# Kernel optimization log

Hardware: AMD Instinct MI355X
Metric: run time of the kernel (lower is better)

Reference implementation:

```python
import jax, jax.numpy as jnp
import numpy as np

DIM = 1024
HEADS = 16
ORDER = 3
B, L = 4, 1024  # note: L must equal DIM due to broadcast in original code


def setup_inputs() -> dict:
    key = jax.random.key(0)
    ks = jax.random.split(key, 10)
    D = DIM
    s = 0.02
    inp = {
        "x": jax.random.normal(ks[0], (B, L, D), dtype=jnp.float32),
        "Wq": jax.random.normal(ks[1], (D, D), dtype=jnp.float32) * s,
        "bq": jnp.zeros((D,), jnp.float32),
        "Wk": jax.random.normal(ks[2], (D, D), dtype=jnp.float32) * s,
        "bk": jnp.zeros((D,), jnp.float32),
        "Wv": jax.random.normal(ks[3], (D, D), dtype=jnp.float32) * s,
        "bv": jnp.zeros((D,), jnp.float32),
        "Wo": jax.random.normal(ks[4], (D, D), dtype=jnp.float32) * s,
        "bo": jnp.zeros((D,), jnp.float32),
        # init per module: zeros field, 0.1 strengths
        "torsion_field": jnp.zeros((ORDER, D), jnp.float32),
        "torsion_strength": jnp.ones((ORDER,), jnp.float32) * 0.1,
    }
    return inp


def reference(x, Wq, bq, Wk, bk, Wv, bv, Wo, bo, torsion_field, torsion_strength):
    Bsz, Ln, D = x.shape
    H = HEADS
    hd = D // H

    def proj(W, b):
        y = jnp.einsum('bld,ed->ble', x, W) + b  # Linear: x @ W.T + b
        return y.reshape(Bsz, Ln, H, hd).transpose(0, 2, 1, 3)  # (B,H,L,hd)

    q = proj(Wq, bq)
    k = proj(Wk, bk)
    v = proj(Wv, bv)

    scores = jnp.einsum('bhld,bhmd->bhlm', q, k) / jnp.sqrt(jnp.float32(hd))

    # torsion bias: sum_i strength_i * sin(arange(L)*(i+1)*pi/L) * sigmoid(field_i)
    # (requires L == D for the elementwise product, as in the original)
    pos = jnp.arange(Ln, dtype=jnp.float32)                       # (L,)
    orders = jnp.arange(1, ORDER + 1, dtype=jnp.float32)          # (O,)
    mods = torsion_strength[:, None] * jnp.sin(pos[None, :] * orders[:, None] * jnp.pi / Ln)  # (O,L)
    phases = jax.nn.sigmoid(torsion_field)                        # (O,D), D==L
    bias = jnp.sum(mods * phases, axis=0)                         # (L,)
    scores = scores + bias[None, None, None, :]

    torsion_energy = jnp.sum(torsion_strength ** 2) / ORDER

    attn = jax.nn.softmax(scores, axis=-1)
    out = jnp.einsum('bhlm,bhmd->bhld', attn, v)
    out = out.transpose(0, 2, 1, 3).reshape(Bsz, Ln, D)
    out = jnp.einsum('bld,ed->ble', out, Wo) + bo
    return out, attn, torsion_energy
```

## Files before the change

### kernel.cpp

```cpp
#include <hip/hip_runtime.h>
#include <hip/hip_bf16.h>

typedef __bf16 bf16x8 __attribute__((ext_vector_type(8)));
typedef float f32x4 __attribute__((ext_vector_type(4)));

#define GLDS16(gp, lp) \
    __builtin_amdgcn_global_load_lds((__attribute__((address_space(1))) void*)(gp), \
                                     (__attribute__((address_space(3))) void*)(lp), 16, 0, 0)

__global__ __launch_bounds__(256) void k_convert(
    const float* __restrict__ x, const float* __restrict__ Wq,
    const float* __restrict__ Wk, const float* __restrict__ Wv,
    const float* __restrict__ Wo,
    __bf16* __restrict__ xb, __bf16* __restrict__ wqb, __bf16* __restrict__ wkb,
    __bf16* __restrict__ wvb, __bf16* __restrict__ wob)
{
    size_t g = (size_t)blockIdx.x * 256 + threadIdx.x;
    size_t e = g * 8;
    const float* src; __bf16* dst; size_t off;
    if (e < 4194304) { src = x; dst = xb; off = e; }
    else {
        size_t t = e - 4194304;
        int w = (int)(t >> 20); off = t & 1048575;
        src = (w == 0 ? Wq : w == 1 ? Wk : w == 2 ? Wv : Wo);
        dst = (w == 0 ? wqb : w == 1 ? wkb : w == 2 ? wvb : wob);
    }
    float4 a = *(const float4*)(src + off);
    float4 b = *(const float4*)(src + off + 4);
    bf16x8 o;
    o[0] = (__bf16)a.x; o[1] = (__bf16)a.y; o[2] = (__bf16)a.z; o[3] = (__bf16)a.w;
    o[4] = (__bf16)b.x; o[5] = (__bf16)b.y; o[6] = (__bf16)b.z; o[7] = (__bf16)b.w;
    *(bf16x8*)(dst + off) = o;
}

__global__ void k_bias(const float* __restrict__ field, const float* __restrict__ strength,
                       float* __restrict__ bias, float* __restrict__ energy_out)
{
    int m = threadIdx.x;
    float acc = 0.f;
    #pragma unroll
    for (int o = 0; o < 3; ++o) {
        float s  = strength[o];
        float ph = 1.f / (1.f + __expf(-field[o * 1024 + m]));
        float t  = (float)(m * (o + 1)) * 3.14159265358979323846f / 1024.f;
        acc += s * sinf(t) * ph;
    }
    bias[m] = acc;
    if (m == 0) {
        float s0 = strength[0], s1 = strength[1], s2 = strength[2];
        energy_out[0] = (s0 * s0 + s1 * s1 + s2 * s2) * (1.f / 3.f);
    }
}

template <int MODE>
__global__ __launch_bounds__(256) void k_gemm(
    const __bf16* __restrict__ A,
    const __bf16* __restrict__ B0, const __bf16* __restrict__ B1, const __bf16* __restrict__ B2,
    const float* __restrict__ bias0, const float* __restrict__ bias1, const float* __restrict__ bias2,
    __bf16* __restrict__ q_ws, __bf16* __restrict__ k_ws, __bf16* __restrict__ vT_ws,
    float* __restrict__ out)
{
    const int K = 1024;
    __shared__ __bf16 As[128 * 32];
    __shared__ __bf16 Bs[128 * 32];

    int tid = threadIdx.x;
    int w = tid >> 6, l = tid & 63;
    int l15 = l & 15, quad = l >> 4;
    int m0 = blockIdx.y * 128, n0 = blockIdx.x * 128;
    int z = blockIdx.z;

    const __bf16* Bm = (MODE == 1) ? B0 : (z == 0 ? B0 : (z == 1 ? B1 : B2));
    const float*  bv = (MODE == 1) ? bias0 : (z == 0 ? bias0 : (z == 1 ? bias1 : bias2));

    int srow = w * 16 + (l >> 2);
    int scol = (l & 3) * 8;
    const __bf16* gA = A  + (size_t)(m0 + srow) * K + scol;
    const __bf16* gB = Bm + (size_t)(n0 + srow) * K + scol;
    __bf16* lA = As + w * 512;
    __bf16* lB = Bs + w * 512;

    f32x4 zero = {0.f, 0.f, 0.f, 0.f};
    f32x4 acc[4][4];
    #pragma unroll
    for (int i = 0; i < 4; ++i)
        #pragma unroll
        for (int j = 0; j < 4; ++j) acc[i][j] = zero;

    int wm = w >> 1, wn = w & 1;

    for (int k0 = 0; k0 < K; k0 += 32) {
        __syncthreads();
        GLDS16(gA + k0,           lA);
        GLDS16(gA + 64 * K + k0,  lA + 2048);
        GLDS16(gB + k0,           lB);
        GLDS16(gB + 64 * K + k0,  lB + 2048);
        __builtin_amdgcn_s_waitcnt(0);
        __syncthreads();

        bf16x8 af[4], bf[4];
        #pragma unroll
        for (int t = 0; t < 4; ++t) {
            af[t] = *(const bf16x8*)&As[(wm * 64 + t * 16 + l15) * 32 + quad * 8];
            bf[t] = *(const bf16x8*)&Bs[(wn * 64 + t * 16 + l15) * 32 + quad * 8];
        }
        #pragma unroll
        for (int i = 0; i < 4; ++i)
            #pragma unroll
            for (int j = 0; j < 4; ++j)
                acc[i][j] = __builtin_amdgcn_mfma_f32_16x16x32_bf16(af[i], bf[j], acc[i][j], 0, 0, 0);
    }

    #pragma unroll
    for (int i = 0; i < 4; ++i) {
        int mbase = m0 + wm * 64 + i * 16 + quad * 4;
        #pragma unroll
        for (int j = 0; j < 4; ++j) {
            int n = n0 + wn * 64 + j * 16 + l15;
            float badd = bv[n];
            #pragma unroll
            for (int r = 0; r < 4; ++r) {
                int m = mbase + r;
                float vres = acc[i][j][r] + badd;
                if (MODE == 1) {
                    out[(size_t)m * 1024 + n] = vres;
                } else {
                    int b = m >> 10, lpos = m & 1023, h = n >> 6, d = n & 63;
                    if (z == 2)
                        vT_ws[(((size_t)(b * 16 + h)) * 64 + d) * 1024 + lpos] = (__bf16)vres;
                    else {
                        __bf16* dst = (z == 0 ? q_ws : k_ws);
                        dst[(((size_t)(b * 16 + h)) * 1024 + lpos) * 64 + d] = (__bf16)vres;
                    }
                }
            }
        }
    }
}

__global__ __launch_bounds__(256) void k_attn(
    const __bf16* __restrict__ qg, const __bf16* __restrict__ kg, const __bf16* __restrict__ vTg,
    const float* __restrict__ bias, float* __restrict__ attn, __bf16* __restrict__ Og)
{
    __shared__ __bf16 q_s[128 * 72];
    __shared__ __bf16 K_s[64 * 72];
    __shared__ __bf16 Vt_s[64 * 72];
    __shared__ __bf16 P_s[128 * 72];
    __shared__ float bias_s[1024];
    __shared__ float rowsum[128];
    __shared__ float rowinv[128];

    int tid = threadIdx.x, w = tid >> 6, l = tid & 63;
    int l15 = l & 15, quad = l >> 4;
    int wm = w >> 1, wn = w & 1;
    int bh = blockIdx.y;
    int m0 = blockIdx.x * 128;

    {
        const __bf16* src = qg + ((size_t)bh * 1024 + m0) * 64;
        for (int i = tid; i < 1024; i += 256) {
            int r = i >> 3, c = (i & 7) * 8;
            *(int4*)&q_s[r * 72 + c] = *(const int4*)&src[(size_t)r * 64 + c];
        }
    }
    *(float4*)&bias_s[tid * 4] = *(const float4*)&bias[tid * 4];
    if (tid < 128) rowsum[tid] = 0.f;

    f32x4 zero = {0.f, 0.f, 0.f, 0.f};
    f32x4 accO[4][2];
    #pragma unroll
    for (int i = 0; i < 4; ++i) { accO[i][0] = zero; accO[i][1] = zero; }

    for (int pass = 0; pass < 2; ++pass) {
        for (int ch = 0; ch < 16; ++ch) {
            int n0c = ch * 64;
            __syncthreads();
            {
                const __bf16* ks = kg + ((size_t)bh * 1024 + n0c) * 64;
                const __bf16* vs = vTg + (size_t)bh * 64 * 1024;
                for (int i = tid; i < 512; i += 256) {
                    int r = i >> 3, c = (i & 7) * 8;
                    *(int4*)&K_s[r * 72 + c] = *(const int4*)&ks[(size_t)r * 64 + c];
                    if (pass == 0)
                        *(int4*)&Vt_s[r * 72 + c] = *(const int4*)&vs[(size_t)r * 1024 + n0c + c];
                }
            }
            __syncthreads();

            f32x4 accS[4][2];
            #pragma unroll
            for (int i = 0; i < 4; ++i) { accS[i][0] = zero; accS[i][1] = zero; }
            #pragma unroll
            for (int ks2 = 0; ks2 < 2; ++ks2) {
                bf16x8 af[4], bf[2];
                #pragma unroll
                for (int t = 0; t < 4; ++t)
                    af[t] = *(const bf16x8*)&q_s[(wm * 64 + t * 16 + l15) * 72 + ks2 * 32 + quad * 8];
                #pragma unroll
                for (int t = 0; t < 2; ++t)
                    bf[t] = *(const bf16x8*)&K_s[(wn * 32 + t * 16 + l15) * 72 + ks2 * 32 + quad * 8];
                #pragma unroll
                for (int i = 0; i < 4; ++i)
                    #pragma unroll
                    for (int j = 0; j < 2; ++j)
                        accS[i][j] = __builtin_amdgcn_mfma_f32_16x16x32_bf16(af[i], bf[j], accS[i][j], 0, 0, 0);
            }

            float p[4][2][4];
            #pragma unroll
            for (int i = 0; i < 4; ++i)
                #pragma unroll
                for (int j = 0; j < 2; ++j) {
                    float bcol = bias_s[n0c + wn * 32 + j * 16 + l15];
                    #pragma unroll
                    for (int r = 0; r < 4; ++r)
                        p[i][j][r] = __expf(0.125f * accS[i][j][r] + bcol);
                }

            if (pass == 0) {
                #pragma unroll
                for (int i = 0; i < 4; ++i)
                    #pragma unroll
                    for (int r = 0; r < 4; ++r) {
                        float s = p[i][0][r] + p[i][1][r];
                        s += __shfl_xor(s, 1, 16);
                        s += __shfl_xor(s, 2, 16);
                        s += __shfl_xor(s, 4, 16);
                        s += __shfl_xor(s, 8, 16);
                        if (l15 == 0) atomicAdd(&rowsum[wm * 64 + i * 16 + quad * 4 + r], s);
                    }
                #pragma unroll
                for (int i = 0; i < 4; ++i)
                    #pragma unroll
                    for (int j = 0; j < 2; ++j)
                        #pragma unroll
                        for (int r = 0; r < 4; ++r)
                            P_s[(wm * 64 + i * 16 + quad * 4 + r) * 72 + wn * 32 + j * 16 + l15] =
                                (__bf16)p[i][j][r];
                __syncthreads();
                #pragma unroll
                for (int ks2 = 0; ks2 < 2; ++ks2) {
                    bf16x8 af[4], bf[2];
                    #pragma unroll
                    for (int t = 0; t < 4; ++t)
                        af[t] = *(const bf16x8*)&P_s[(wm * 64 + t * 16 + l15) * 72 + ks2 * 32 + quad * 8];
                    #pragma unroll
                    for (int t = 0; t < 2; ++t)
                        bf[t] = *(const bf16x8*)&Vt_s[(wn * 32 + t * 16 + l15) * 72 + ks2 * 32 + quad * 8];
                    #pragma unroll
                    for (int i = 0; i < 4; ++i)
                        #pragma unroll
                        for (int j = 0; j < 2; ++j)
                            accO[i][j] = __builtin_amdgcn_mfma_f32_16x16x32_bf16(af[i], bf[j], accO[i][j], 0, 0, 0);
                }
            } else {
                float* dst = attn + ((size_t)bh << 20) + (size_t)m0 * 1024;
                #pragma unroll
                for (int i = 0; i < 4; ++i)
                    #pragma unroll
                    for (int r = 0; r < 4; ++r) {
                        int row = wm * 64 + i * 16 + quad * 4 + r;
                        float inv = rowinv[row];
                        #pragma unroll
                        for (int j = 0; j < 2; ++j) {
                            int col = n0c + wn * 32 + j * 16 + l15;
                            dst[(size_t)row * 1024 + col] = p[i][j][r] * inv;
                        }
                    }
            }
        }
        if (pass == 0) {
            __syncthreads();
            if (tid < 128) rowinv[tid] = 1.f / rowsum[tid];
            __syncthreads();
            int b = bh >> 4, h = bh & 15;
            #pragma unroll
            for (int i = 0; i < 4; ++i)
                #pragma unroll
                for (int r = 0; r < 4; ++r) {
                    int row = wm * 64 + i * 16 + quad * 4 + r;
                    float inv = rowinv[row];
                    #pragma unroll
                    for (int j = 0; j < 2; ++j) {
                        int d = wn * 32 + j * 16 + l15;
                        Og[((size_t)(b * 1024 + m0 + row)) * 1024 + h * 64 + d] =
                            (__bf16)(accO[i][j][r] * inv);
                    }
                }
        }
    }
}

extern "C" void kernel_launch(void* const* d_in, const int* in_sizes, int n_in,
                              void* d_out, int out_size, void* d_ws, size_t ws_size,
                              hipStream_t stream)
{
    const float* x  = (const float*)d_in[0];
    const float* Wq = (const float*)d_in[1];
    const float* bq = (const float*)d_in[2];
    const float* Wk = (const float*)d_in[3];
    const float* bk = (const float*)d_in[4];
    const float* Wv = (const float*)d_in[5];
    const float* bvv= (const float*)d_in[6];
    const float* Wo = (const float*)d_in[7];
    const float* bo = (const float*)d_in[8];
    const float* tf = (const float*)d_in[9];
    const float* ts = (const float*)d_in[10];

    float* out    = (float*)d_out;
    float* attn   = out + 4194304;
    float* energy = attn + 67108864;

    char* ws = (char*)d_ws;
    float*  bias  = (float*)ws;
    __bf16* xb    = (__bf16*)(ws + 4096);
    __bf16* wqb   = (__bf16*)(ws + 4096 + 8388608);
    __bf16* wkb   = wqb + 1048576;
    __bf16* wvb   = wkb + 1048576;
    __bf16* wob   = wvb + 1048576;
    __bf16* q_ws  = wob + 1048576;
    __bf16* k_ws  = q_ws + 4194304;
    __bf16* vT_ws = k_ws + 4194304;
    __bf16* O_ws  = xb;

    k_convert<<<dim3(4096), dim3(256), 0, stream>>>(x, Wq, Wk, Wv, Wo, xb, wqb, wkb, wvb, wob);
    k_bias<<<dim3(1), dim3(1024), 0, stream>>>(tf, ts, bias, energy);
    k_gemm<0><<<dim3(8, 32, 3), dim3(256), 0, stream>>>(xb, wqb, wkb, wvb, bq, bk, bvv,
                                                        q_ws, k_ws, vT_ws, nullptr);
    k_attn<<<dim3(8, 64), dim3(256), 0, stream>>>(q_ws, k_ws, vT_ws, bias, attn, O_ws);
    k_gemm<1><<<dim3(8, 32, 1), dim3(256), 0, stream>>>(O_ws, wob, nullptr, nullptr, bo,
                                                        nullptr, nullptr, nullptr, nullptr,
                                                        nullptr, out);
}
```

Baseline: 492.8 us.

## Prefetch K/V into registers in attention, fuse bias kernel, retile output GEMM

The attention kernel now register-prefetches the next K/V chunk while the current one is computed. It replaces plain syncthreads with barriers that only wait on LDS counters, accumulates row sums in registers instead of doing per-chunk LDS atomics, raises wave priority around the MFMA blocks, and sets launch bounds for two blocks per CU. Separately, the bias/energy computation is folded into an extra block of the convert kernel to save a launch, and the output projection GEMM uses a 64-wide N tile so it launches twice as many blocks. These changes target global-load latency, barrier stalls and low occupancy, at the cost of higher register pressure.

```diff
diff --git a/kernel.cpp b/kernel.cpp
--- a/kernel.cpp
+++ b/kernel.cpp
@@ -7,14 +7,43 @@
 #define GLDS16(gp, lp) \
     __builtin_amdgcn_global_load_lds((__attribute__((address_space(1))) void*)(gp), \
                                      (__attribute__((address_space(3))) void*)(lp), 16, 0, 0)
+
+static __device__ __forceinline__ void bar_nodrain() {
+    __builtin_amdgcn_sched_barrier(0);
+    asm volatile("s_waitcnt lgkmcnt(0)" ::: "memory");
+    __builtin_amdgcn_s_barrier();
+    __builtin_amdgcn_sched_barrier(0);
+}
 
 __global__ __launch_bounds__(256) void k_convert(
     const float* __restrict__ x, const float* __restrict__ Wq,
     const float* __restrict__ Wk, const float* __restrict__ Wv,
     const float* __restrict__ Wo,
     __bf16* __restrict__ xb, __bf16* __restrict__ wqb, __bf16* __restrict__ wkb,
-    __bf16* __restrict__ wvb, __bf16* __restrict__ wob)
+    __bf16* __restrict__ wvb, __bf16* __restrict__ wob,
+    const float* __restrict__ field, const float* __restrict__ strength,
+    float* __restrict__ bias_out, float* __restrict__ energy_out)
 {
+    if (blockIdx.x == 4096) {
+        int t = threadIdx.x;
+        #pragma unroll
+        for (int m = t; m < 1024; m += 256) {
+            float acc = 0.f;
+            #pragma unroll
+            for (int o = 0; o < 3; ++o) {
+                float s  = strength[o];
+                float ph = 1.f / (1.f + __expf(-field[o * 1024 + m]));
+                float tt = (float)(m * (o + 1)) * 3.14159265358979323846f / 1024.f;
+                acc += s * sinf(tt) * ph;
+            }
+            bias_out[m] = acc;
+        }
+        if (t == 0) {
+            float s0 = strength[0], s1 = strength[1], s2 = strength[2];
+            energy_out[0] = (s0 * s0 + s1 * s1 + s2 * s2) * (1.f / 3.f);
+        }
+        return;
+    }
     size_t g = (size_t)blockIdx.x * 256 + threadIdx.x;
     size_t e = g * 8;
     const float* src; __bf16* dst; size_t off;
@@ -33,26 +62,7 @@
     *(bf16x8*)(dst + off) = o;
 }
 
-__global__ void k_bias(const float* __restrict__ field, const float* __restrict__ strength,
-                       float* __restrict__ bias, float* __restrict__ energy_out)
-{
-    int m = threadIdx.x;
-    float acc = 0.f;
-    #pragma unroll
-    for (int o = 0; o < 3; ++o) {
-        float s  = strength[o];
-        float ph = 1.f / (1.f + __expf(-field[o * 1024 + m]));
-        float t  = (float)(m * (o + 1)) * 3.14159265358979323846f / 1024.f;
-        acc += s * sinf(t) * ph;
-    }
-    bias[m] = acc;
-    if (m == 0) {
-        float s0 = strength[0], s1 = strength[1], s2 = strength[2];
-        energy_out[0] = (s0 * s0 + s1 * s1 + s2 * s2) * (1.f / 3.f);
-    }
-}
-
-template <int MODE>
+template <int MODE, int BN>
 __global__ __launch_bounds__(256) void k_gemm(
     const __bf16* __restrict__ A,
     const __bf16* __restrict__ B0, const __bf16* __restrict__ B1, const __bf16* __restrict__ B2,
@@ -61,13 +71,14 @@
     float* __restrict__ out)
 {
     const int K = 1024;
+    constexpr int NB = BN / 32;
     __shared__ __bf16 As[128 * 32];
-    __shared__ __bf16 Bs[128 * 32];
+    __shared__ __bf16 Bs[BN * 32];
 
     int tid = threadIdx.x;
     int w = tid >> 6, l = tid & 63;
     int l15 = l & 15, quad = l >> 4;
-    int m0 = blockIdx.y * 128, n0 = blockIdx.x * 128;
+    int m0 = blockIdx.y * 128, n0 = blockIdx.x * BN;
     int z = blockIdx.z;
 
     const __bf16* Bm = (MODE == 1) ? B0 : (z == 0 ? B0 : (z == 1 ? B1 : B2));
@@ -81,11 +92,11 @@
     __bf16* lB = Bs + w * 512;
 
     f32x4 zero = {0.f, 0.f, 0.f, 0.f};
-    f32x4 acc[4][4];
+    f32x4 acc[4][NB];
     #pragma unroll
     for (int i = 0; i < 4; ++i)
         #pragma unroll
-        for (int j = 0; j < 4; ++j) acc[i][j] = zero;
+        for (int j = 0; j < NB; ++j) acc[i][j] = zero;
 
     int wm = w >> 1, wn = w & 1;
 
@@ -94,29 +105,30 @@
         GLDS16(gA + k0,           lA);
         GLDS16(gA + 64 * K + k0,  lA + 2048);
         GLDS16(gB + k0,           lB);
-        GLDS16(gB + 64 * K + k0,  lB + 2048);
+        if (BN == 128) GLDS16(gB + 64 * K + k0,  lB + 2048);
         __builtin_amdgcn_s_waitcnt(0);
         __syncthreads();
 
-        bf16x8 af[4], bf[4];
-        #pragma unroll
-        for (int t = 0; t < 4; ++t) {
+        bf16x8 af[4], bfr[NB];
+        #pragma unroll
+        for (int t = 0; t < 4; ++t)
             af[t] = *(const bf16x8*)&As[(wm * 64 + t * 16 + l15) * 32 + quad * 8];
-            bf[t] = *(const bf16x8*)&Bs[(wn * 64 + t * 16 + l15) * 32 + quad * 8];
-        }
+        #pragma unroll
+        for (int t = 0; t < NB; ++t)
+            bfr[t] = *(const bf16x8*)&Bs[(wn * (BN / 2) + t * 16 + l15) * 32 + quad * 8];
         #pragma unroll
         for (int i = 0; i < 4; ++i)
             #pragma unroll
-            for (int j = 0; j < 4; ++j)
-                acc[i][j] = __builtin_amdgcn_mfma_f32_16x16x32_bf16(af[i], bf[j], acc[i][j], 0, 0, 0);
+            for (int j = 0; j < NB; ++j)
+                acc[i][j] = __builtin_amdgcn_mfma_f32_16x16x32_bf16(af[i], bfr[j], acc[i][j], 0, 0, 0);
     }
 
     #pragma unroll
     for (int i = 0; i < 4; ++i) {
         int mbase = m0 + wm * 64 + i * 16 + quad * 4;
         #pragma unroll
-        for (int j = 0; j < 4; ++j) {
-            int n = n0 + wn * 64 + j * 16 + l15;
+        for (int j = 0; j < NB; ++j) {
+            int n = n0 + wn * (BN / 2) + j * 16 + l15;
             float badd = bv[n];
             #pragma unroll
             for (int r = 0; r < 4; ++r) {
@@ -138,7 +150,7 @@
     }
 }
 
-__global__ __launch_bounds__(256) void k_attn(
+__global__ __launch_bounds__(256, 2) void k_attn(
     const __bf16* __restrict__ qg, const __bf16* __restrict__ kg, const __bf16* __restrict__ vTg,
     const float* __restrict__ bias, float* __restrict__ attn, __bf16* __restrict__ Og)
 {
@@ -166,45 +178,71 @@
     *(float4*)&bias_s[tid * 4] = *(const float4*)&bias[tid * 4];
     if (tid < 128) rowsum[tid] = 0.f;
 
+    int sr = tid >> 3;
+    int sc = (tid & 7) * 8;
+    const __bf16* kbase = kg  + (size_t)bh * 1024 * 64;
+    const __bf16* vbase = vTg + (size_t)bh * 64 * 1024;
+
+    int4 kr0 = *(const int4*)&kbase[(size_t)(sr)      * 64 + sc];
+    int4 kr1 = *(const int4*)&kbase[(size_t)(sr + 32) * 64 + sc];
+    int4 vr0 = *(const int4*)&vbase[(size_t)(sr)      * 1024 + sc];
+    int4 vr1 = *(const int4*)&vbase[(size_t)(sr + 32) * 1024 + sc];
+
     f32x4 zero = {0.f, 0.f, 0.f, 0.f};
     f32x4 accO[4][2];
     #pragma unroll
     for (int i = 0; i < 4; ++i) { accO[i][0] = zero; accO[i][1] = zero; }
+    float rs[4][4];
+    #pragma unroll
+    for (int i = 0; i < 4; ++i)
+        #pragma unroll
+        for (int r = 0; r < 4; ++r) rs[i][r] = 0.f;
 
     for (int pass = 0; pass < 2; ++pass) {
         for (int ch = 0; ch < 16; ++ch) {
             int n0c = ch * 64;
-            __syncthreads();
-            {
-                const __bf16* ks = kg + ((size_t)bh * 1024 + n0c) * 64;
-                const __bf16* vs = vTg + (size_t)bh * 64 * 1024;
-                for (int i = tid; i < 512; i += 256) {
-                    int r = i >> 3, c = (i & 7) * 8;
-                    *(int4*)&K_s[r * 72 + c] = *(const int4*)&ks[(size_t)r * 64 + c];
-                    if (pass == 0)
-                        *(int4*)&Vt_s[r * 72 + c] = *(const int4*)&vs[(size_t)r * 1024 + n0c + c];
-                }
-            }
-            __syncthreads();
+            bar_nodrain();
+            *(int4*)&K_s[sr * 72 + sc]        = kr0;
+            *(int4*)&K_s[(sr + 32) * 72 + sc] = kr1;
+            if (pass == 0) {
+                *(int4*)&Vt_s[sr * 72 + sc]        = vr0;
+                *(int4*)&Vt_s[(sr + 32) * 72 + sc] = vr1;
+            }
+            bar_nodrain();
+
+            if (ch < 15) {
+                int nn = n0c + 64;
+                kr0 = *(const int4*)&kbase[(size_t)(nn + sr)      * 64 + sc];
+                kr1 = *(const int4*)&kbase[(size_t)(nn + sr + 32) * 64 + sc];
+                if (pass == 0) {
+                    vr0 = *(const int4*)&vbase[(size_t)(sr)      * 1024 + nn + sc];
+                    vr1 = *(const int4*)&vbase[(size_t)(sr + 32) * 1024 + nn + sc];
+                }
+            } else if (pass == 0) {
+                kr0 = *(const int4*)&kbase[(size_t)(sr)      * 64 + sc];
+                kr1 = *(const int4*)&kbase[(size_t)(sr + 32) * 64 + sc];
+            }
 
             f32x4 accS[4][2];
             #pragma unroll
             for (int i = 0; i < 4; ++i) { accS[i][0] = zero; accS[i][1] = zero; }
+            __builtin_amdgcn_s_setprio(1);
             #pragma unroll
             for (int ks2 = 0; ks2 < 2; ++ks2) {
-                bf16x8 af[4], bf[2];
+                bf16x8 af[4], bfr[2];
                 #pragma unroll
                 for (int t = 0; t < 4; ++t)
                     af[t] = *(const bf16x8*)&q_s[(wm * 64 + t * 16 + l15) * 72 + ks2 * 32 + quad * 8];
                 #pragma unroll
                 for (int t = 0; t < 2; ++t)
-                    bf[t] = *(const bf16x8*)&K_s[(wn * 32 + t * 16 + l15) * 72 + ks2 * 32 + quad * 8];
+                    bfr[t] = *(const bf16x8*)&K_s[(wn * 32 + t * 16 + l15) * 72 + ks2 * 32 + quad * 8];
                 #pragma unroll
                 for (int i = 0; i < 4; ++i)
                     #pragma unroll
                     for (int j = 0; j < 2; ++j)
-                        accS[i][j] = __builtin_amdgcn_mfma_f32_16x16x32_bf16(af[i], bf[j], accS[i][j], 0, 0, 0);
-            }
+                        accS[i][j] = __builtin_amdgcn_mfma_f32_16x16x32_bf16(af[i], bfr[j], accS[i][j], 0, 0, 0);
+            }
+            __builtin_amdgcn_s_setprio(0);
 
             float p[4][2][4];
             #pragma unroll
@@ -221,14 +259,8 @@
                 #pragma unroll
                 for (int i = 0; i < 4; ++i)
                     #pragma unroll
-                    for (int r = 0; r < 4; ++r) {
-                        float s = p[i][0][r] + p[i][1][r];
-                        s += __shfl_xor(s, 1, 16);
-                        s += __shfl_xor(s, 2, 16);
-                        s += __shfl_xor(s, 4, 16);
-                        s += __shfl_xor(s, 8, 16);
-                        if (l15 == 0) atomicAdd(&rowsum[wm * 64 + i * 16 + quad * 4 + r], s);
-                    }
+                    for (int r = 0; r < 4; ++r)
+                        rs[i][r] += p[i][0][r] + p[i][1][r];
                 #pragma unroll
                 for (int i = 0; i < 4; ++i)
                     #pragma unroll
@@ -237,22 +269,24 @@
                         for (int r = 0; r < 4; ++r)
                             P_s[(wm * 64 + i * 16 + quad * 4 + r) * 72 + wn * 32 + j * 16 + l15] =
                                 (__bf16)p[i][j][r];
-                __syncthreads();
+                bar_nodrain();
+                __builtin_amdgcn_s_setprio(1);
                 #pragma unroll
                 for (int ks2 = 0; ks2 < 2; ++ks2) {
-                    bf16x8 af[4], bf[2];
+                    bf16x8 af[4], bfr[2];
                     #pragma unroll
                     for (int t = 0; t < 4; ++t)
                         af[t] = *(const bf16x8*)&P_s[(wm * 64 + t * 16 + l15) * 72 + ks2 * 32 + quad * 8];
                     #pragma unroll
                     for (int t = 0; t < 2; ++t)
-                        bf[t] = *(const bf16x8*)&Vt_s[(wn * 32 + t * 16 + l15) * 72 + ks2 * 32 + quad * 8];
+                        bfr[t] = *(const bf16x8*)&Vt_s[(wn * 32 + t * 16 + l15) * 72 + ks2 * 32 + quad * 8];
                     #pragma unroll
                     for (int i = 0; i < 4; ++i)
                         #pragma unroll
                         for (int j = 0; j < 2; ++j)
-                            accO[i][j] = __builtin_amdgcn_mfma_f32_16x16x32_bf16(af[i], bf[j], accO[i][j], 0, 0, 0);
-                }
+                            accO[i][j] = __builtin_amdgcn_mfma_f32_16x16x32_bf16(af[i], bfr[j], accO[i][j], 0, 0, 0);
+                }
+                __builtin_amdgcn_s_setprio(0);
             } else {
                 float* dst = attn + ((size_t)bh << 20) + (size_t)m0 * 1024;
                 #pragma unroll
@@ -270,9 +304,20 @@
             }
         }
         if (pass == 0) {
-            __syncthreads();
+            #pragma unroll
+            for (int i = 0; i < 4; ++i)
+                #pragma unroll
+                for (int r = 0; r < 4; ++r) {
+                    float s = rs[i][r];
+                    s += __shfl_xor(s, 1, 16);
+                    s += __shfl_xor(s, 2, 16);
+                    s += __shfl_xor(s, 4, 16);
+                    s += __shfl_xor(s, 8, 16);
+                    if (l15 == 0) atomicAdd(&rowsum[wm * 64 + i * 16 + quad * 4 + r], s);
+                }
+            bar_nodrain();
             if (tid < 128) rowinv[tid] = 1.f / rowsum[tid];
-            __syncthreads();
+            bar_nodrain();
             int b = bh >> 4, h = bh & 15;
             #pragma unroll
             for (int i = 0; i < 4; ++i)
@@ -323,12 +368,12 @@
     __bf16* vT_ws = k_ws + 4194304;
     __bf16* O_ws  = xb;
 
-    k_convert<<<dim3(4096), dim3(256), 0, stream>>>(x, Wq, Wk, Wv, Wo, xb, wqb, wkb, wvb, wob);
-    k_bias<<<dim3(1), dim3(1024), 0, stream>>>(tf, ts, bias, energy);
-    k_gemm<0><<<dim3(8, 32, 3), dim3(256), 0, stream>>>(xb, wqb, wkb, wvb, bq, bk, bvv,
-                                                        q_ws, k_ws, vT_ws, nullptr);
+    k_convert<<<dim3(4097), dim3(256), 0, stream>>>(x, Wq, Wk, Wv, Wo, xb, wqb, wkb, wvb, wob,
+                                                    tf, ts, bias, energy);
+    k_gemm<0, 128><<<dim3(8, 32, 3), dim3(256), 0, stream>>>(xb, wqb, wkb, wvb, bq, bk, bvv,
+                                                             q_ws, k_ws, vT_ws, nullptr);
     k_attn<<<dim3(8, 64), dim3(256), 0, stream>>>(q_ws, k_ws, vT_ws, bias, attn, O_ws);
-    k_gemm<1><<<dim3(8, 32, 1), dim3(256), 0, stream>>>(O_ws, wob, nullptr, nullptr, bo,
-                                                        nullptr, nullptr, nullptr, nullptr,
-                                                        nullptr, out);
-}
+    k_gemm<1, 64><<<dim3(16, 32, 1), dim3(256), 0, stream>>>(O_ws, wob, nullptr, nullptr, bo,
+                                                             nullptr, nullptr, nullptr, nullptr,
+                                                             nullptr, out);
+}
```

Measured after the change: 434.0 us. 1.14x faster.
